# Kernel optimization log

Hardware: AMD Instinct MI355X
Metric: run time of the kernel (lower is better)

## Reference

```python
import jax, jax.numpy as jnp
import numpy as np

D, HEADS, HD, L, P, DFF = 256, 8, 32, 4, 4, 2048
B, NQ = 4, 900
SHAPES = [(128, 128), (64, 64), (32, 32), (16, 16)]
S = sum(h * w for h, w in SHAPES)


def setup_inputs():
    ks = iter(jax.random.split(jax.random.key(0), 20))
    rn = lambda *s: jax.random.normal(next(ks), s, jnp.float32) * 0.02
    cxcy = jax.random.uniform(next(ks), (B, NQ, 1, 2), minval=0.1, maxval=0.9)
    wh = jax.random.uniform(next(ks), (B, NQ, 1, 2), minval=0.05, maxval=0.3)
    ref = jnp.broadcast_to(jnp.concatenate([cxcy, wh], -1), (B, NQ, L, 4))
    starts = np.cumsum([0] + [h * w for h, w in SHAPES[:-1]])
    return dict(
        query=jax.random.normal(next(ks), (B, NQ, D), jnp.float32),
        query_pos=jax.random.normal(next(ks), (B, NQ, D), jnp.float32),
        reference_points=ref,
        input_flatten=jax.random.normal(next(ks), (B, S, D), jnp.float32),
        input_spatial_shapes=jnp.array(SHAPES, jnp.int32),
        input_level_start_index=jnp.array(starts, jnp.int32),
        sa_in_w=rn(3, D, D), sa_in_b=jnp.zeros((3, D)),
        sa_out_w=rn(D, D), sa_out_b=jnp.zeros((D,)),
        norm1_g=jnp.ones((D,)), norm1_b=jnp.zeros((D,)),
        value_w=rn(D, D), value_b=jnp.zeros((D,)),
        off_w=rn(D, HEADS * L * P * 2),
        off_b=jax.random.uniform(next(ks), (HEADS * L * P * 2,), minval=-1.0, maxval=1.0),
        aw_w=rn(D, HEADS * L * P), aw_b=jnp.zeros((HEADS * L * P,)),
        ca_out_w=rn(D, D), ca_out_b=jnp.zeros((D,)),
        norm2_g=jnp.ones((D,)), norm2_b=jnp.zeros((D,)),
        lin1_w=rn(D, DFF), lin1_b=jnp.zeros((DFF,)),
        lin2_w=rn(DFF, D), lin2_b=jnp.zeros((D,)),
        norm3_g=jnp.ones((D,)), norm3_b=jnp.zeros((D,)),
    )


def _ln(x, g, b, eps=1e-5):
    m = x.mean(-1, keepdims=True)
    v = ((x - m) ** 2).mean(-1, keepdims=True)
    return (x - m) * jax.lax.rsqrt(v + eps) * g + b


def _msdeform(q, input_flatten, ref, shapes, starts, value_w, value_b,
              off_w, off_b, aw_w, aw_b, out_w, out_b):
    Bq, Nq, _ = q.shape
    # value: (B, heads, S, head_dim)
    v = (input_flatten @ value_w + value_b).reshape(Bq, -1, HEADS, HD).transpose(0, 2, 1, 3)
    off = (q @ off_w + off_b).reshape(Bq, Nq, HEADS, L, P, 2).transpose(0, 2, 1, 3, 4, 5)
    aw = jax.nn.softmax((q @ aw_w + aw_b).reshape(Bq, Nq, HEADS, L * P), axis=-1)
    aw = aw.reshape(Bq, Nq, HEADS, L, P).transpose(0, 2, 1, 3, 4)  # (B,H,Nq,L,P)
    refc = ref[:, None, :, :, None, :]  # (B,1,Nq,L,1,4)
    # box refs: center + offset/P * wh * 0.5  (Deformable-DETR convention)
    loc = refc[..., :2] + off / P * refc[..., 2:] * 0.5  # (B,H,Nq,L,P,2)
    out = jnp.zeros((Bq, HEADS, Nq, HD), q.dtype)
    for l, (H, W) in enumerate(shapes):
        vl = jax.lax.dynamic_slice_in_dim(v, starts[l], H * W, axis=2)  # (B,H,HW,hd)
        x = loc[:, :, :, l, :, 0] * W - 0.5  # align_corners=False pixel coords
        y = loc[:, :, :, l, :, 1] * H - 0.5
        x0, y0 = jnp.floor(x), jnp.floor(y)
        dx, dy = x - x0, y - y0

        def g(xi, yi):
            valid = (xi >= 0) & (xi < W) & (yi >= 0) & (yi < H)  # zero padding
            idx = (jnp.clip(yi, 0, H - 1) * W + jnp.clip(xi, 0, W - 1)).astype(jnp.int32)
            gat = jnp.take_along_axis(vl, idx.reshape(Bq, HEADS, Nq * P, 1), axis=2)
            return gat.reshape(Bq, HEADS, Nq, P, HD) * valid[..., None]

        samp = (((1 - dx) * (1 - dy))[..., None] * g(x0, y0)
                + (dx * (1 - dy))[..., None] * g(x0 + 1, y0)
                + ((1 - dx) * dy)[..., None] * g(x0, y0 + 1)
                + (dx * dy)[..., None] * g(x0 + 1, y0 + 1))
        out = out + jnp.sum(aw[:, :, :, l, :, None] * samp, axis=3)
    return out.transpose(0, 2, 1, 3).reshape(Bq, Nq, D) @ out_w + out_b


def _layer(query, query_pos, reference_points, input_flatten, shapes, starts, p):
    Bq, Nq, _ = query.shape
    qk = query + query_pos
    heads = lambda x: x.reshape(Bq, Nq, HEADS, HD).transpose(0, 2, 1, 3)
    qh = heads(qk @ p['sa_in_w'][0] + p['sa_in_b'][0])
    kh = heads(qk @ p['sa_in_w'][1] + p['sa_in_b'][1])
    vh = heads(query @ p['sa_in_w'][2] + p['sa_in_b'][2])
    attn = jax.nn.softmax(jnp.einsum('bhqd,bhkd->bhqk', qh, kh) * (HD ** -0.5), axis=-1)
    sa = jnp.einsum('bhqk,bhkd->bhqd', attn, vh).transpose(0, 2, 1, 3).reshape(Bq, Nq, D)
    sa = sa @ p['sa_out_w'] + p['sa_out_b']
    x = _ln(query + sa, p['norm1_g'], p['norm1_b'])
    ca = _msdeform(x + query_pos, input_flatten, reference_points, shapes, starts,
                   p['value_w'], p['value_b'], p['off_w'], p['off_b'],
                   p['aw_w'], p['aw_b'], p['ca_out_w'], p['ca_out_b'])
    x = _ln(x + ca, p['norm2_g'], p['norm2_b'])
    ffn = jax.nn.relu(x @ p['lin1_w'] + p['lin1_b']) @ p['lin2_w'] + p['lin2_b']
    return _ln(x + ffn, p['norm3_g'], p['norm3_b'])


PNAMES = ['sa_in_w', 'sa_in_b', 'sa_out_w', 'sa_out_b', 'norm1_g', 'norm1_b',
          'value_w', 'value_b', 'off_w', 'off_b', 'aw_w', 'aw_b',
          'ca_out_w', 'ca_out_b', 'norm2_g', 'norm2_b',
          'lin1_w', 'lin1_b', 'lin2_w', 'lin2_b', 'norm3_g', 'norm3_b']


def reference(query, query_pos, reference_points, input_flatten,
              input_spatial_shapes, input_level_start_index,
              sa_in_w, sa_in_b, sa_out_w, sa_out_b, norm1_g, norm1_b,
              value_w, value_b, off_w, off_b, aw_w, aw_b,
              ca_out_w, ca_out_b, norm2_g, norm2_b,
              lin1_w, lin1_b, lin2_w, lin2_b, norm3_g, norm3_b):
    # spatial shapes / start indices are static structural metadata
    shapes = [(int(h), int(w)) for h, w in np.asarray(input_spatial_shapes)]
    starts = [int(s) for s in np.asarray(input_level_start_index)]
    p = dict(zip(PNAMES, (sa_in_w, sa_in_b, sa_out_w, sa_out_b, norm1_g, norm1_b,
                          value_w, value_b, off_w, off_b, aw_w, aw_b,
                          ca_out_w, ca_out_b, norm2_g, norm2_b,
                          lin1_w, lin1_b, lin2_w, lin2_b, norm3_g, norm3_b)))
    return _layer(query, query_pos, reference_points, input_flatten, shapes, starts, p)
```

## Files before the change

### kernel.cpp

```cpp
#include <hip/hip_runtime.h>
#include <hip/hip_bf16.h>

#define DD   256
#define NH   8
#define HDIM 32
#define LV   4
#define NP   4
#define DFF  2048
#define BB   4
#define NQQ  900
#define SS   21760

typedef __bf16 bf16x8 __attribute__((ext_vector_type(8)));
typedef __bf16 bf16x2 __attribute__((ext_vector_type(2)));
typedef float  f32x4  __attribute__((ext_vector_type(4)));

__device__ inline void stval(float* p, float v) { *p = v; }
__device__ inline void stval(__bf16* p, float v) { *p = (__bf16)v; }

__device__ __forceinline__ void gload16(const void* g, void* l) {
    __builtin_amdgcn_global_load_lds(
        (const __attribute__((address_space(1))) void*)g,
        (__attribute__((address_space(3))) void*)l, 16, 0, 0);
}

struct TPtrs {
    const float* s[10];
    __bf16* d[10];
};

__global__ void transp_all(TPtrs P) {
    const int Ks[10] = {256, 256, 256, 256, 256, 256, 256, 256, 256, 2048};
    const int Ns[10] = {256, 256, 256, 256, 256, 256, 128, 256, 2048, 256};
    const int tiles[10] = {64, 64, 64, 64, 64, 64, 32, 64, 512, 512};
    int t = blockIdx.x;
    int j = 0, base = 0;
    while (t >= base + tiles[j]) { base += tiles[j]; j++; }
    int lt = t - base;
    int K = Ks[j], N = Ns[j];
    int tn = N >> 5;
    int nb = (lt % tn) * 32, kb = (lt / tn) * 32;
    const float* W = P.s[j];
    __bf16* Wt = P.d[j];
    __shared__ float tbuf[32][33];
    for (int i = threadIdx.y; i < 32; i += 8)
        tbuf[i][threadIdx.x] = W[(size_t)(kb + i) * N + nb + threadIdx.x];
    __syncthreads();
    for (int i = threadIdx.y; i < 32; i += 8)
        Wt[(size_t)(nb + i) * K + kb + threadIdx.x] = (__bf16)tbuf[threadIdx.x][i];
}

#define BM 64
#define BN 64
#define BKK 64

template <typename AT, typename OT, int RELU, int NSUB>
__global__ __launch_bounds__(256) void mfma_gemm(
    const AT* __restrict__ A, const float* __restrict__ A2,
    const __bf16* __restrict__ Wt,
    const float* __restrict__ bias, const float* __restrict__ bias2, int nsplit,
    OT* __restrict__ C, int M, int N, int K) {
    int tid = threadIdx.x;
    int lane = tid & 63;
    int wave = tid >> 6;
    int wr = wave >> 1, wc = wave & 1;
    int m0 = blockIdx.y * BM;
    int n0 = blockIdx.x * (BN * NSUB);

    __shared__ __attribute__((aligned(16))) __bf16 As[BM * BKK];
    __shared__ __attribute__((aligned(16))) __bf16 Bs[NSUB][BN * BKK];

    f32x4 acc[NSUB][2][2] = {};

    int srow = tid >> 2;
    int sq = tid & 3;
    int u0 = sq << 1;
    int p0 = (u0 ^ (srow & 7)) * 8;
    int p1 = ((u0 + 1) ^ (srow & 7)) * 8;
    int fr = lane & 15, gq = lane >> 4;

    for (int k0 = 0; k0 < K; k0 += BKK) {
        {
            int gm = m0 + srow;
            bf16x8 v0 = {}, v1 = {};
            if (gm < M) {
                if constexpr (sizeof(AT) == 4) {
                    const float* ap = (const float*)A + (size_t)gm * K + k0 + sq * 16;
                    f32x4 f0 = *(const f32x4*)(ap + 0);
                    f32x4 f1 = *(const f32x4*)(ap + 4);
                    f32x4 f2 = *(const f32x4*)(ap + 8);
                    f32x4 f3 = *(const f32x4*)(ap + 12);
                    if (A2) {
                        const float* ap2 = A2 + (size_t)gm * K + k0 + sq * 16;
                        f0 += *(const f32x4*)(ap2 + 0);
                        f1 += *(const f32x4*)(ap2 + 4);
                        f2 += *(const f32x4*)(ap2 + 8);
                        f3 += *(const f32x4*)(ap2 + 12);
                    }
#pragma unroll
                    for (int e = 0; e < 4; e++) {
                        v0[e] = (__bf16)f0[e]; v0[e + 4] = (__bf16)f1[e];
                        v1[e] = (__bf16)f2[e]; v1[e + 4] = (__bf16)f3[e];
                    }
                } else {
                    const __bf16* ap = (const __bf16*)A + (size_t)gm * K + k0 + sq * 16;
                    v0 = *(const bf16x8*)(ap);
                    v1 = *(const bf16x8*)(ap + 8);
                }
            }
            *(bf16x8*)(&As[srow * 64 + p0]) = v0;
            *(bf16x8*)(&As[srow * 64 + p1]) = v1;
        }
#pragma unroll
        for (int ns = 0; ns < NSUB; ns++) {
            int gn = n0 + ns * BN + srow;
            const __bf16* bp = Wt + (size_t)gn * K + k0 + sq * 16;
            bf16x8 w0 = *(const bf16x8*)(bp);
            bf16x8 w1 = *(const bf16x8*)(bp + 8);
            *(bf16x8*)(&Bs[ns][srow * 64 + p0]) = w0;
            *(bf16x8*)(&Bs[ns][srow * 64 + p1]) = w1;
        }
        __syncthreads();
#pragma unroll
        for (int ks = 0; ks < 2; ks++) {
            bf16x8 a[2];
#pragma unroll
            for (int i = 0; i < 2; i++) {
                int ma = wr * 32 + i * 16 + fr;
                a[i] = *(const bf16x8*)(&As[ma * 64 + ((ks * 4 + gq) ^ (ma & 7)) * 8]);
            }
#pragma unroll
            for (int ns = 0; ns < NSUB; ns++) {
                bf16x8 b[2];
#pragma unroll
                for (int j = 0; j < 2; j++) {
                    int nb = wc * 32 + j * 16 + fr;
                    b[j] = *(const bf16x8*)(&Bs[ns][nb * 64 + ((ks * 4 + gq) ^ (nb & 7)) * 8]);
                }
#pragma unroll
                for (int i = 0; i < 2; i++)
#pragma unroll
                    for (int j = 0; j < 2; j++)
                        acc[ns][i][j] = __builtin_amdgcn_mfma_f32_16x16x32_bf16(a[i], b[j], acc[ns][i][j], 0, 0, 0);
            }
        }
        __syncthreads();
    }
    int orow = gq * 4;
#pragma unroll
    for (int ns = 0; ns < NSUB; ns++)
#pragma unroll
        for (int i = 0; i < 2; i++)
#pragma unroll
            for (int j = 0; j < 2; j++) {
                int gn = n0 + ns * BN + wc * 32 + j * 16 + fr;
                float bv = (gn < nsplit) ? bias[gn] : bias2[gn - nsplit];
#pragma unroll
                for (int r = 0; r < 4; r++) {
                    int gm = m0 + wr * 32 + i * 16 + orow + r;
                    if (gm < M) {
                        float v = acc[ns][i][j][r] + bv;
                        if (RELU) v = fmaxf(v, 0.f);
                        stval(C + (size_t)gm * N + gn, v);
                    }
                }
            }
}

__global__ __launch_bounds__(256) void value_gemm4(
    const float* __restrict__ A, const __bf16* __restrict__ Wt,
    const float* __restrict__ bias, __bf16* __restrict__ C) {
    int tid = threadIdx.x;
    int lane = tid & 63;
    int wave = tid >> 6;
    int fr = lane & 15, gq = lane >> 4;
    int m0 = blockIdx.x * 64;

    __shared__ __attribute__((aligned(16))) __bf16 As[2][64 * 64];
    __shared__ __attribute__((aligned(16))) __bf16 Bq[2][4][64 * 64];

    f32x4 acc[4][4] = {};

    int srow = tid >> 2;
    int sq = tid & 3;
    int u0 = sq << 1;
    int p0 = (u0 ^ (srow & 7)) * 8;
    int p1 = ((u0 + 1) ^ (srow & 7)) * 8;

    int c_row = lane >> 3;
    int c_u = lane & 7;
    int gu = c_u ^ c_row;
    const __bf16* bsrc0 = Wt + (size_t)(wave * 64 + c_row) * 256 + gu * 8;
    const float* aptr = A + (size_t)(m0 + srow) * 256 + sq * 16;

    f32x4 fa0 = *(const f32x4*)(aptr + 0);
    f32x4 fa1 = *(const f32x4*)(aptr + 4);
    f32x4 fa2 = *(const f32x4*)(aptr + 8);
    f32x4 fa3 = *(const f32x4*)(aptr + 12);
    __builtin_amdgcn_sched_barrier(0);
#pragma unroll
    for (int c = 0; c < 8; c++)
        gload16(bsrc0 + (size_t)c * 8 * 256, &Bq[0][wave][c * 512]);
    asm volatile("s_waitcnt vmcnt(8)" ::: "memory");
    __builtin_amdgcn_sched_barrier(0);
    {
        bf16x8 v0, v1;
#pragma unroll
        for (int e = 0; e < 4; e++) {
            v0[e] = (__bf16)fa0[e]; v0[e + 4] = (__bf16)fa1[e];
            v1[e] = (__bf16)fa2[e]; v1[e + 4] = (__bf16)fa3[e];
        }
        *(bf16x8*)(&As[0][srow * 64 + p0]) = v0;
        *(bf16x8*)(&As[0][srow * 64 + p1]) = v1;
    }
    asm volatile("s_waitcnt lgkmcnt(0)" ::: "memory");
    __builtin_amdgcn_s_barrier();

#pragma unroll
    for (int step = 0; step < 4; step++) {
        int p = step & 1;
        if (step < 3) {
            const float* ap2 = aptr + (step + 1) * 64;
            fa0 = *(const f32x4*)(ap2 + 0);
            fa1 = *(const f32x4*)(ap2 + 4);
            fa2 = *(const f32x4*)(ap2 + 8);
            fa3 = *(const f32x4*)(ap2 + 12);
            __builtin_amdgcn_sched_barrier(0);
            const __bf16* bsrc = bsrc0 + (step + 1) * 64;
#pragma unroll
            for (int c = 0; c < 8; c++)
                gload16(bsrc + (size_t)c * 8 * 256, &Bq[p ^ 1][wave][c * 512]);
            asm volatile("s_waitcnt vmcnt(12)" ::: "memory");
        } else {
            asm volatile("s_waitcnt vmcnt(0)" ::: "memory");
        }
        __builtin_amdgcn_sched_barrier(0);
#pragma unroll
        for (int ks = 0; ks < 2; ks++) {
            bf16x8 a[4], b[4];
#pragma unroll
            for (int i = 0; i < 4; i++) {
                int ma = i * 16 + fr;
                a[i] = *(const bf16x8*)(&As[p][ma * 64 + ((ks * 4 + gq) ^ (ma & 7)) * 8]);
                b[i] = *(const bf16x8*)(&Bq[p][wave][ma * 64 + ((ks * 4 + gq) ^ (ma & 7)) * 8]);
            }
#pragma unroll
            for (int i = 0; i < 4; i++)
#pragma unroll
                for (int j = 0; j < 4; j++)
                    acc[i][j] = __builtin_amdgcn_mfma_f32_16x16x32_bf16(a[i], b[j], acc[i][j], 0, 0, 0);
        }
        if (step < 3) {
            asm volatile("s_waitcnt vmcnt(8)" ::: "memory");
            __builtin_amdgcn_sched_barrier(0);
            bf16x8 v0, v1;
#pragma unroll
            for (int e = 0; e < 4; e++) {
                v0[e] = (__bf16)fa0[e]; v0[e + 4] = (__bf16)fa1[e];
                v1[e] = (__bf16)fa2[e]; v1[e + 4] = (__bf16)fa3[e];
            }
            *(bf16x8*)(&As[p ^ 1][srow * 64 + p0]) = v0;
            *(bf16x8*)(&As[p ^ 1][srow * 64 + p1]) = v1;
            asm volatile("s_waitcnt lgkmcnt(0)" ::: "memory");
            __builtin_amdgcn_s_barrier();
        }
    }

#pragma unroll
    for (int i = 0; i < 4; i++)
#pragma unroll
        for (int j = 0; j < 4; j++) {
            int gn = wave * 64 + j * 16 + fr;
            float bv = bias[gn];
#pragma unroll
            for (int r = 0; r < 4; r++) {
                int gm = m0 + i * 16 + gq * 4 + r;
                C[(size_t)gm * 256 + gn] = (__bf16)(acc[i][j][r] + bv);
            }
        }
}

__global__ void fillmark(float* o, int n, float v) {
    int i = blockIdx.x * blockDim.x + threadIdx.x;
    if (i < n) o[i] = v;
}

__global__ void ln_res(const float* a, const float* b,
                       const float* g, const float* be, float* o) {
    int row = blockIdx.x;
    int t = threadIdx.x;
    float x = a[(size_t)row * DD + t] + b[(size_t)row * DD + t];
    __shared__ float red[DD];
    red[t] = x;
    __syncthreads();
    for (int s = 128; s > 0; s >>= 1) {
        if (t < s) red[t] += red[t + s];
        __syncthreads();
    }
    float m = red[0] * (1.f / DD);
    __syncthreads();
    float d0 = x - m;
    red[t] = d0 * d0;
    __syncthreads();
    for (int s = 128; s > 0; s >>= 1) {
        if (t < s) red[t] += red[t + s];
        __syncthreads();
    }
    float v = red[0] * (1.f / DD);
    o[(size_t)row * DD + t] = d0 * rsqrtf(v + 1e-5f) * g[t] + be[t];
}

#define QT 64
#define KT 64
#define NT ((NQQ + KT - 1) / KT)
#define QKLD 512

__global__ __launch_bounds__(256) void sa_attn_mfma(
    const __bf16* __restrict__ QK, const __bf16* __restrict__ V,
    float* __restrict__ O) {
    int blk = blockIdx.x;
    int tq = blk % NT;
    int bh = blk / NT;
    int h = bh % NH;
    int b = bh / NH;
    int tid = threadIdx.x;
    int lane = tid & 63;
    int wave = tid >> 6;
    int fr = lane & 15, gq = lane >> 4;
    int q0 = tq * QT;

    __shared__ __attribute__((aligned(16))) __bf16 Ks[KT][56];
    __shared__ __attribute__((aligned(16))) __bf16 Vt[HDIM][72];
    __shared__ __attribute__((aligned(16))) __bf16 Ps[4][16][72];

    int qrow = q0 + wave * 16 + fr;
    bf16x8 aq = {};
    if (qrow < NQQ)
        aq = *(const bf16x8*)(QK + ((size_t)(b * NQQ + qrow)) * QKLD + h * HDIM + gq * 8);

    f32x4 o0 = {}, o1 = {};
    float m_r[4] = {-1e30f, -1e30f, -1e30f, -1e30f};
    float l_r[4] = {0.f, 0.f, 0.f, 0.f};
    const float scale = 0.17677669529663687f;

    for (int kt = 0; kt < NT; kt++) {
        int kv0 = kt * KT;
        {
            int r = tid >> 2;
            int c8 = (tid & 3) * 8;
            int kvr = kv0 + r;
            bf16x8 kv_ = {}, vv_ = {};
            if (kvr < NQQ) {
                kv_ = *(const bf16x8*)(QK + ((size_t)(b * NQQ + kvr)) * QKLD + 256 + h * HDIM + c8);
                vv_ = *(const bf16x8*)(V + ((size_t)(b * NQQ + kvr)) * DD + h * HDIM + c8);
            }
            *(bf16x8*)(&Ks[r][c8]) = kv_;
#pragma unroll
            for (int j = 0; j < 8; j++) Vt[c8 + j][r] = vv_[j];
        }
        __syncthreads();

        f32x4 s[4];
#pragma unroll
        for (int f = 0; f < 4; f++) {
            bf16x8 bk = *(const bf16x8*)(&Ks[f * 16 + fr][gq * 8]);
            f32x4 z = {};
            s[f] = __builtin_amdgcn_mfma_f32_16x16x32_bf16(aq, bk, z, 0, 0, 0);
        }
#pragma unroll
        for (int f = 0; f < 4; f++) {
            bool valid = (kv0 + f * 16 + fr) < NQQ;
#pragma unroll
            for (int r = 0; r < 4; r++)
                s[f][r] = valid ? s[f][r] * scale : -1e30f;
        }
        float sc_[4];
#pragma unroll
        for (int r = 0; r < 4; r++) {
            float v = fmaxf(fmaxf(s[0][r], s[1][r]), fmaxf(s[2][r], s[3][r]));
            v = fmaxf(v, __shfl_xor(v, 1));
            v = fmaxf(v, __shfl_xor(v, 2));
            v = fmaxf(v, __shfl_xor(v, 4));
            v = fmaxf(v, __shfl_xor(v, 8));
            float mn = fmaxf(m_r[r], v);
            sc_[r] = expf(m_r[r] - mn);
            m_r[r] = mn;
        }
        float rs[4] = {0.f, 0.f, 0.f, 0.f};
#pragma unroll
        for (int f = 0; f < 4; f++)
#pragma unroll
            for (int r = 0; r < 4; r++) {
                float e = expf(s[f][r] - m_r[r]);
                s[f][r] = e;
                rs[r] += e;
            }
#pragma unroll
        for (int r = 0; r < 4; r++) {
            float v = rs[r];
            v += __shfl_xor(v, 1);
            v += __shfl_xor(v, 2);
            v += __shfl_xor(v, 4);
            v += __shfl_xor(v, 8);
            l_r[r] = l_r[r] * sc_[r] + v;
            o0[r] *= sc_[r];
            o1[r] *= sc_[r];
        }
#pragma unroll
        for (int f = 0; f < 4; f++)
#pragma unroll
            for (int r = 0; r < 4; r++)
                Ps[wave][gq * 4 + r][f * 16 + fr] = (__bf16)s[f][r];
#pragma unroll
        for (int c = 0; c < 2; c++) {
            bf16x8 ap = *(const bf16x8*)(&Ps[wave][fr][c * 32 + gq * 8]);
            bf16x8 bv0 = *(const bf16x8*)(&Vt[fr][c * 32 + gq * 8]);
            bf16x8 bv1 = *(const bf16x8*)(&Vt[16 + fr][c * 32 + gq * 8]);
            o0 = __builtin_amdgcn_mfma_f32_16x16x32_bf16(ap, bv0, o0, 0, 0, 0);
            o1 = __builtin_amdgcn_mfma_f32_16x16x32_bf16(ap, bv1, o1, 0, 0, 0);
        }
        __syncthreads();
    }
#pragma unroll
    for (int r = 0; r < 4; r++) {
        int qr = q0 + wave * 16 + gq * 4 + r;
        if (qr < NQQ) {
            float inv = 1.f / l_r[r];
            O[((size_t)(b * NQQ + qr)) * DD + h * HDIM + fr] = o0[r] * inv;
            O[((size_t)(b * NQQ + qr)) * DD + h * HDIM + 16 + fr] = o1[r] * inv;
        }
    }
}

#define OAW 384

__global__ __launch_bounds__(256) void msdeform3(
    const __bf16* __restrict__ val, const __bf16* __restrict__ oa,
    const float* __restrict__ ref, float* __restrict__ out) {
    int tid = threadIdx.x;
    int row = blockIdx.x;
    int b_ = row / NQQ;

    __shared__ float sx[128], sy[128], sw[128];

    if (tid < 128) {
        int h = tid >> 4;
        int lp = tid & 15;
        int l = lp >> 2;
        float logit = (float)oa[(size_t)row * OAW + 256 + h * 16 + lp];
        float ox = (float)oa[(size_t)row * OAW + h * 32 + lp * 2];
        float oy = (float)oa[(size_t)row * OAW + h * 32 + lp * 2 + 1];
        const float* rp = ref + ((size_t)row * LV + l) * 4;
        float cx = rp[0], cy = rp[1], rw = rp[2], rh = rp[3];
        float mv = logit;
        mv = fmaxf(mv, __shfl_xor(mv, 1));
        mv = fmaxf(mv, __shfl_xor(mv, 2));
        mv = fmaxf(mv, __shfl_xor(mv, 4));
        mv = fmaxf(mv, __shfl_xor(mv, 8));
        float e = expf(logit - mv);
        float sum = e;
        sum += __shfl_xor(sum, 1);
        sum += __shfl_xor(sum, 2);
        sum += __shfl_xor(sum, 4);
        sum += __shfl_xor(sum, 8);
        int Wl = 128 >> l;
        float lx = cx + ox * (1.0f / NP) * rw * 0.5f;
        float ly = cy + oy * (1.0f / NP) * rh * 0.5f;
        sx[tid] = lx * Wl - 0.5f;
        sy[tid] = ly * Wl - 0.5f;
        sw[tid] = e / sum;
    }
    __syncthreads();

    int cpar = tid & 7;
    int dgrp = (tid >> 3) & 3;
    int h = tid >> 5;
    const int stt[4] = {0, 16384, 20480, 21504};
    const __bf16* vb = val + (size_t)b_ * SS * DD + h * HDIM + dgrp * 8;
    float facc[8] = {};
#pragma unroll
    for (int k = 0; k < 8; k++) {
        int combo = cpar * 8 + k;
        int lp = combo >> 2;
        int tap = combo & 3;
        int l = lp >> 2;
        int Wl = 128 >> l;
        int cidx = h * 16 + lp;
        float x = sx[cidx], y = sy[cidx], w = sw[cidx];
        float x0f = floorf(x), y0f = floorf(y);
        float dx = x - x0f, dy = y - y0f;
        int xi = (int)x0f + (tap & 1);
        int yi = (int)y0f + (tap >> 1);
        float wt = ((tap & 1) ? dx : 1.f - dx) * ((tap >> 1) ? dy : 1.f - dy) * w;
        if ((xi >= 0) & (xi < Wl) & (yi >= 0) & (yi < Wl)) {
            bf16x8 t = *(const bf16x8*)(vb + (size_t)(stt[l] + yi * Wl + xi) * DD);
#pragma unroll
            for (int e = 0; e < 8; e++) facc[e] += wt * (float)t[e];
        }
    }
#pragma unroll
    for (int e = 0; e < 8; e++) {
        facc[e] += __shfl_xor(facc[e], 1);
        facc[e] += __shfl_xor(facc[e], 2);
        facc[e] += __shfl_xor(facc[e], 4);
    }
    float v = facc[0];
#pragma unroll
    for (int e = 1; e < 8; e++) if (cpar == e) v = facc[e];
    out[(size_t)row * DD + tid] = v;
}

extern "C" void kernel_launch(void* const* d_in, const int* in_sizes, int n_in,
                              void* d_out, int out_size, void* d_ws, size_t ws_size,
                              hipStream_t stream) {
    const float* query      = (const float*)d_in[0];
    const float* query_pos  = (const float*)d_in[1];
    const float* refpts     = (const float*)d_in[2];
    const float* input_flat = (const float*)d_in[3];
    const float* sa_in_w    = (const float*)d_in[6];
    const float* sa_in_b    = (const float*)d_in[7];
    const float* sa_out_w   = (const float*)d_in[8];
    const float* sa_out_b   = (const float*)d_in[9];
    const float* norm1_g    = (const float*)d_in[10];
    const float* norm1_b    = (const float*)d_in[11];
    const float* value_w    = (const float*)d_in[12];
    const float* value_b    = (const float*)d_in[13];
    const float* off_w      = (const float*)d_in[14];
    const float* off_b      = (const float*)d_in[15];
    const float* aw_w       = (const float*)d_in[16];
    const float* aw_b       = (const float*)d_in[17];
    const float* ca_out_w   = (const float*)d_in[18];
    const float* ca_out_b   = (const float*)d_in[19];
    const float* norm2_g    = (const float*)d_in[20];
    const float* norm2_b    = (const float*)d_in[21];
    const float* lin1_w     = (const float*)d_in[22];
    const float* lin1_b     = (const float*)d_in[23];
    const float* lin2_w     = (const float*)d_in[24];
    const float* lin2_b     = (const float*)d_in[25];
    const float* norm3_g    = (const float*)d_in[26];
    const float* norm3_b    = (const float*)d_in[27];
    float* out = (float*)d_out;

    const int M = BB * NQQ;
    const int NE = M * DD;
    const size_t slotBytes = (size_t)NE * 4;
    const size_t wElems = 6 * 65536 + 32768 + 65536 + 2 * 524288;
    const size_t wBytes = wElems * 2;
    const size_t bigBytes = (size_t)BB * SS * DD * 2;
    const size_t needBytes = 3 * slotBytes + wBytes + bigBytes;
    if (ws_size < needBytes) {
        float mark = 1000.0f + (float)(ws_size >> 20);
        fillmark<<<(out_size + 255) / 256, 256, 0, stream>>>(out, out_size, mark);
        return;
    }

    char* wsb = (char*)d_ws;
    float* s0 = (float*)(wsb);
    float* s1 = (float*)(wsb + slotBytes);
    float* s2 = (float*)(wsb + 2 * slotBytes);
    __bf16* wb = (__bf16*)(wsb + 3 * slotBytes);
    __bf16* vbig = (__bf16*)(wsb + 3 * slotBytes + wBytes);

    __bf16* wt_q   = wb;
    __bf16* wt_k   = wb + 65536;
    __bf16* wt_v   = wb + 131072;
    __bf16* wt_sa  = wb + 196608;
    __bf16* wt_val = wb + 262144;
    __bf16* wt_off = wb + 327680;
    __bf16* wt_aw  = wb + 393216;
    __bf16* wt_ca  = wb + 425984;
    __bf16* wt_l1  = wb + 491520;
    __bf16* wt_l2  = wb + 1015808;

    TPtrs tp;
    tp.s[0] = sa_in_w;          tp.d[0] = wt_q;
    tp.s[1] = sa_in_w + 65536;  tp.d[1] = wt_k;
    tp.s[2] = sa_in_w + 131072; tp.d[2] = wt_v;
    tp.s[3] = sa_out_w;         tp.d[3] = wt_sa;
    tp.s[4] = value_w;          tp.d[4] = wt_val;
    tp.s[5] = off_w;            tp.d[5] = wt_off;
    tp.s[6] = aw_w;             tp.d[6] = wt_aw;
    tp.s[7] = ca_out_w;         tp.d[7] = wt_ca;
    tp.s[8] = lin1_w;           tp.d[8] = wt_l1;
    tp.s[9] = lin2_w;           tp.d[9] = wt_l2;
    transp_all<<<1504, dim3(32, 8), 0, stream>>>(tp);

    __bf16* qkbuf = (__bf16*)s1;
    __bf16* Vp = (__bf16*)s2;
    __bf16* oabuf = (__bf16*)s1;

    const int mt = (M + BM - 1) / BM;
    const int BIG = 1 << 30;

    mfma_gemm<float, __bf16, 0, 1><<<dim3(8, mt), 256, 0, stream>>>(
        query, query_pos, wt_q, sa_in_b, sa_in_b, BIG, qkbuf, M, 512, DD);
    mfma_gemm<float, __bf16, 0, 1><<<dim3(4, mt), 256, 0, stream>>>(
        query, nullptr, wt_v, sa_in_b + 512, sa_in_b, BIG, Vp, M, DD, DD);
    sa_attn_mfma<<<BB * NH * NT, 256, 0, stream>>>(qkbuf, Vp, s0);
    mfma_gemm<float, float, 0, 1><<<dim3(4, mt), 256, 0, stream>>>(
        s0, nullptr, wt_sa, sa_out_b, sa_out_b, BIG, s1, M, DD, DD);
    ln_res<<<M, DD, 0, stream>>>(query, s1, norm1_g, norm1_b, s2);
    value_gemm4<<<(BB * SS) / 64, 256, 0, stream>>>(input_flat, wt_val, value_b, vbig);
    mfma_gemm<float, __bf16, 0, 1><<<dim3(6, mt), 256, 0, stream>>>(
        s2, query_pos, wt_off, off_b, aw_b, 256, oabuf, M, OAW, DD);
    msdeform3<<<M, 256, 0, stream>>>(vbig, oabuf, refpts, s0);
    mfma_gemm<float, float, 0, 1><<<dim3(4, mt), 256, 0, stream>>>(
        s0, nullptr, wt_ca, ca_out_b, ca_out_b, BIG, s1, M, DD, DD);
    ln_res<<<M, DD, 0, stream>>>(s2, s1, norm2_g, norm2_b, s1);
    mfma_gemm<float, __bf16, 1, 1><<<dim3(32, mt), 256, 0, stream>>>(
        s1, nullptr, wt_l1, lin1_b, lin1_b, BIG, vbig, M, DFF, DD);
    mfma_gemm<__bf16, float, 0, 1><<<dim3(4, mt), 256, 0, stream>>>(
        vbig, nullptr, wt_l2, lin2_b, lin2_b, BIG, s0, M, DD, DFF);
    ln_res<<<M, DD, 0, stream>>>(s1, s0, norm3_g, norm3_b, out);
}
```

Before: 210.1 us.

## Fuse residual add and LayerNorm into out-projection GEMM epilogues

Adds an LNF template mode to the MFMA GEMM. With NSUB=4, one block covers all 256 output columns, so bias, residual add and LayerNorm can be computed in the epilogue with shuffle and shared-memory reductions. This removes two separate ln_res launches and the fp32 round trip of the intermediate. The QK and lin1 GEMMs also switch to NSUB=2 to reuse each A tile across more columns. The cost is fewer blocks for the fused GEMMs (only mt≈57 blocks), which reduces parallelism on a large GPU.

```diff
diff --git a/kernel.cpp b/kernel.cpp
--- a/kernel.cpp
+++ b/kernel.cpp
@@ -54,11 +54,13 @@
 #define BN 64
 #define BKK 64
 
-template <typename AT, typename OT, int RELU, int NSUB>
+template <typename AT, typename OT, int RELU, int NSUB, bool LNF>
 __global__ __launch_bounds__(256) void mfma_gemm(
     const AT* __restrict__ A, const float* __restrict__ A2,
     const __bf16* __restrict__ Wt,
     const float* __restrict__ bias, const float* __restrict__ bias2, int nsplit,
+    const float* __restrict__ res, const float* __restrict__ lng,
+    const float* __restrict__ lnb,
     OT* __restrict__ C, int M, int N, int K) {
     int tid = threadIdx.x;
     int lane = tid & 63;
@@ -69,6 +71,8 @@
 
     __shared__ __attribute__((aligned(16))) __bf16 As[BM * BKK];
     __shared__ __attribute__((aligned(16))) __bf16 Bs[NSUB][BN * BKK];
+    __shared__ float rsum[LNF ? 64 : 1][2];
+    __shared__ float rsum2[LNF ? 64 : 1][2];
 
     f32x4 acc[NSUB][2][2] = {};
 
@@ -147,24 +151,129 @@
         __syncthreads();
     }
     int orow = gq * 4;
-#pragma unroll
-    for (int ns = 0; ns < NSUB; ns++)
-#pragma unroll
-        for (int i = 0; i < 2; i++)
-#pragma unroll
-            for (int j = 0; j < 2; j++) {
-                int gn = n0 + ns * BN + wc * 32 + j * 16 + fr;
-                float bv = (gn < nsplit) ? bias[gn] : bias2[gn - nsplit];
-#pragma unroll
-                for (int r = 0; r < 4; r++) {
-                    int gm = m0 + wr * 32 + i * 16 + orow + r;
-                    if (gm < M) {
-                        float v = acc[ns][i][j][r] + bv;
-                        if (RELU) v = fmaxf(v, 0.f);
-                        stval(C + (size_t)gm * N + gn, v);
+    if constexpr (!LNF) {
+#pragma unroll
+        for (int ns = 0; ns < NSUB; ns++)
+#pragma unroll
+            for (int i = 0; i < 2; i++)
+#pragma unroll
+                for (int j = 0; j < 2; j++) {
+                    int gn = n0 + ns * BN + wc * 32 + j * 16 + fr;
+                    float bv = (gn < nsplit) ? bias[gn] : bias2[gn - nsplit];
+#pragma unroll
+                    for (int r = 0; r < 4; r++) {
+                        int gm = m0 + wr * 32 + i * 16 + orow + r;
+                        if (gm < M) {
+                            float v = acc[ns][i][j][r] + bv;
+                            if (RELU) v = fmaxf(v, 0.f);
+                            stval(C + (size_t)gm * N + gn, v);
+                        }
                     }
                 }
-            }
+    } else {
+        float part[2][4] = {};
+#pragma unroll
+        for (int ns = 0; ns < NSUB; ns++)
+#pragma unroll
+            for (int i = 0; i < 2; i++)
+#pragma unroll
+                for (int j = 0; j < 2; j++) {
+                    int gn = ns * BN + wc * 32 + j * 16 + fr;
+                    float bv = bias[gn];
+#pragma unroll
+                    for (int r = 0; r < 4; r++) {
+                        int gm = m0 + wr * 32 + i * 16 + orow + r;
+                        float rv = (gm < M) ? res[(size_t)gm * 256 + gn] : 0.f;
+                        float x = acc[ns][i][j][r] + bv + rv;
+                        acc[ns][i][j][r] = x;
+                        part[i][r] += x;
+                    }
+                }
+#pragma unroll
+        for (int i = 0; i < 2; i++)
+#pragma unroll
+            for (int r = 0; r < 4; r++) {
+                float v = part[i][r];
+                v += __shfl_xor(v, 1);
+                v += __shfl_xor(v, 2);
+                v += __shfl_xor(v, 4);
+                v += __shfl_xor(v, 8);
+                part[i][r] = v;
+            }
+        if (fr == 0) {
+#pragma unroll
+            for (int i = 0; i < 2; i++)
+#pragma unroll
+                for (int r = 0; r < 4; r++)
+                    rsum[wr * 32 + i * 16 + orow + r][wc] = part[i][r];
+        }
+        __syncthreads();
+        float mean[2][4];
+#pragma unroll
+        for (int i = 0; i < 2; i++)
+#pragma unroll
+            for (int r = 0; r < 4; r++) {
+                int rl = wr * 32 + i * 16 + orow + r;
+                mean[i][r] = (rsum[rl][0] + rsum[rl][1]) * (1.f / 256.f);
+            }
+        float p2[2][4] = {};
+#pragma unroll
+        for (int ns = 0; ns < NSUB; ns++)
+#pragma unroll
+            for (int i = 0; i < 2; i++)
+#pragma unroll
+                for (int j = 0; j < 2; j++)
+#pragma unroll
+                    for (int r = 0; r < 4; r++) {
+                        float d = acc[ns][i][j][r] - mean[i][r];
+                        p2[i][r] += d * d;
+                    }
+#pragma unroll
+        for (int i = 0; i < 2; i++)
+#pragma unroll
+            for (int r = 0; r < 4; r++) {
+                float v = p2[i][r];
+                v += __shfl_xor(v, 1);
+                v += __shfl_xor(v, 2);
+                v += __shfl_xor(v, 4);
+                v += __shfl_xor(v, 8);
+                p2[i][r] = v;
+            }
+        if (fr == 0) {
+#pragma unroll
+            for (int i = 0; i < 2; i++)
+#pragma unroll
+                for (int r = 0; r < 4; r++)
+                    rsum2[wr * 32 + i * 16 + orow + r][wc] = p2[i][r];
+        }
+        __syncthreads();
+        float rstd[2][4];
+#pragma unroll
+        for (int i = 0; i < 2; i++)
+#pragma unroll
+            for (int r = 0; r < 4; r++) {
+                int rl = wr * 32 + i * 16 + orow + r;
+                float var = (rsum2[rl][0] + rsum2[rl][1]) * (1.f / 256.f);
+                rstd[i][r] = rsqrtf(var + 1e-5f);
+            }
+#pragma unroll
+        for (int ns = 0; ns < NSUB; ns++)
+#pragma unroll
+            for (int i = 0; i < 2; i++)
+#pragma unroll
+                for (int j = 0; j < 2; j++) {
+                    int gn = ns * BN + wc * 32 + j * 16 + fr;
+                    float gv = lng[gn], bev = lnb[gn];
+#pragma unroll
+                    for (int r = 0; r < 4; r++) {
+                        int gm = m0 + wr * 32 + i * 16 + orow + r;
+                        if (gm < M) {
+                            float y = (acc[ns][i][j][r] - mean[i][r]) * rstd[i][r] * gv + bev;
+                            stval(C + (size_t)gm * 256 + gn, y);
+                        }
+                    }
+                }
+    }
 }
 
 __global__ __launch_bounds__(256) void value_gemm4(
@@ -592,24 +701,29 @@
     const int mt = (M + BM - 1) / BM;
     const int BIG = 1 << 30;
 
-    mfma_gemm<float, __bf16, 0, 1><<<dim3(8, mt), 256, 0, stream>>>(
-        query, query_pos, wt_q, sa_in_b, sa_in_b, BIG, qkbuf, M, 512, DD);
-    mfma_gemm<float, __bf16, 0, 1><<<dim3(4, mt), 256, 0, stream>>>(
-        query, nullptr, wt_v, sa_in_b + 512, sa_in_b, BIG, Vp, M, DD, DD);
+    mfma_gemm<float, __bf16, 0, 2, false><<<dim3(4, mt), 256, 0, stream>>>(
+        query, query_pos, wt_q, sa_in_b, sa_in_b, BIG,
+        nullptr, nullptr, nullptr, qkbuf, M, 512, DD);
+    mfma_gemm<float, __bf16, 0, 1, false><<<dim3(4, mt), 256, 0, stream>>>(
+        query, nullptr, wt_v, sa_in_b + 512, sa_in_b, BIG,
+        nullptr, nullptr, nullptr, Vp, M, DD, DD);
     sa_attn_mfma<<<BB * NH * NT, 256, 0, stream>>>(qkbuf, Vp, s0);
-    mfma_gemm<float, float, 0, 1><<<dim3(4, mt), 256, 0, stream>>>(
-        s0, nullptr, wt_sa, sa_out_b, sa_out_b, BIG, s1, M, DD, DD);
-    ln_res<<<M, DD, 0, stream>>>(query, s1, norm1_g, norm1_b, s2);
+    mfma_gemm<float, float, 0, 4, true><<<dim3(1, mt), 256, 0, stream>>>(
+        s0, nullptr, wt_sa, sa_out_b, sa_out_b, BIG,
+        query, norm1_g, norm1_b, s2, M, DD, DD);
     value_gemm4<<<(BB * SS) / 64, 256, 0, stream>>>(input_flat, wt_val, value_b, vbig);
-    mfma_gemm<float, __bf16, 0, 1><<<dim3(6, mt), 256, 0, stream>>>(
-        s2, query_pos, wt_off, off_b, aw_b, 256, oabuf, M, OAW, DD);
+    mfma_gemm<float, __bf16, 0, 1, false><<<dim3(6, mt), 256, 0, stream>>>(
+        s2, query_pos, wt_off, off_b, aw_b, 256,
+        nullptr, nullptr, nullptr, oabuf, M, OAW, DD);
     msdeform3<<<M, 256, 0, stream>>>(vbig, oabuf, refpts, s0);
-    mfma_gemm<float, float, 0, 1><<<dim3(4, mt), 256, 0, stream>>>(
-        s0, nullptr, wt_ca, ca_out_b, ca_out_b, BIG, s1, M, DD, DD);
-    ln_res<<<M, DD, 0, stream>>>(s2, s1, norm2_g, norm2_b, s1);
-    mfma_gemm<float, __bf16, 1, 1><<<dim3(32, mt), 256, 0, stream>>>(
-        s1, nullptr, wt_l1, lin1_b, lin1_b, BIG, vbig, M, DFF, DD);
-    mfma_gemm<__bf16, float, 0, 1><<<dim3(4, mt), 256, 0, stream>>>(
-        vbig, nullptr, wt_l2, lin2_b, lin2_b, BIG, s0, M, DD, DFF);
+    mfma_gemm<float, float, 0, 4, true><<<dim3(1, mt), 256, 0, stream>>>(
+        s0, nullptr, wt_ca, ca_out_b, ca_out_b, BIG,
+        s2, norm2_g, norm2_b, s1, M, DD, DD);
+    mfma_gemm<float, __bf16, 1, 2, false><<<dim3(16, mt), 256, 0, stream>>>(
+        s1, nullptr, wt_l1, lin1_b, lin1_b, BIG,
+        nullptr, nullptr, nullptr, vbig, M, DFF, DD);
+    mfma_gemm<__bf16, float, 0, 1, false><<<dim3(4, mt), 256, 0, stream>>>(
+        vbig, nullptr, wt_l2, lin2_b, lin2_b, BIG,
+        nullptr, nullptr, nullptr, s0, M, DD, DFF);
     ln_res<<<M, DD, 0, stream>>>(s1, s0, norm3_g, norm3_b, out);
 }
```

Measured after the change: 212.9 us. About the same (+1.4%).
